# Kernel optimization log

Hardware: AMD Instinct MI355X
Metric: run time of the kernel (lower is better)

## Reference

```python
import jax, jax.numpy as jnp
import numpy as np

NUM_CODES = 1296
D_DIM = 64


def setup_inputs() -> dict:
    key = jax.random.key(0)
    k1, k2 = jax.random.split(key)
    inputs = jax.random.normal(k1, (32, 64, 64, D_DIM), dtype=jnp.float32)
    # lecun_normal init: stddev = 1/sqrt(fan_in) with fan_in = d
    embeddings = jax.random.normal(k2, (NUM_CODES, D_DIM), dtype=jnp.float32) / np.sqrt(D_DIM)
    return {"inputs": inputs, "embeddings": embeddings}


def reference(inputs, embeddings):
    x1 = jnp.sum(inputs ** 2, axis=-1, keepdims=True)          # [b,m,n,1]
    x2 = jnp.sum(embeddings ** 2, axis=-1)                      # [k]
    x3 = jnp.einsum('bmnd,kd->bmnk', inputs, embeddings)        # [b,m,n,k]
    D = x1 + x2 - 2.0 * x3
    codes = jnp.argmin(D, axis=-1).astype(jnp.int32)            # [b,m,n]
    code_vecs = embeddings[codes]                               # [b,m,n,d]
    return codes, code_vecs
```

## Files before the change

kernel.cpp:

```cpp
#include <hip/hip_runtime.h>

#define NUM_CODES 1296
#define PAD_CODES 1344
#define DDIM 64
#define NUM_Q 131072
#define THREADS 256
#define QPW 32
#define QPB 128
#define MARGIN 0.25f
#define SLOTS 24
#define CHUNK 96
#define NSTEP 14

typedef __attribute__((ext_vector_type(8))) short bf16x8;
typedef __attribute__((ext_vector_type(4))) float f32x4;

__device__ __forceinline__ ushort f2bf(float f) {
    unsigned u = __float_as_uint(f);
    return (ushort)((u + 0x7fffu + ((u >> 16) & 1u)) >> 16);
}

__global__ __launch_bounds__(64) void vq_prep(const float* __restrict__ emb,
                                              float* __restrict__ enorm,
                                              ushort* __restrict__ eh) {
    int k = blockIdx.x * 64 + threadIdx.x;
    if (k >= PAD_CODES) return;
    int ks = k < NUM_CODES ? k : NUM_CODES - 1;
    const float* e = emb + (size_t)ks * DDIM;
    float f[DDIM];
#pragma unroll
    for (int i = 0; i < 16; ++i) {
        float4 v = *(const float4*)(e + 4 * i);
        f[4*i] = v.x; f[4*i+1] = v.y; f[4*i+2] = v.z; f[4*i+3] = v.w;
    }
    {
#pragma clang fp contract(off)
        float r8[8];
#pragma unroll
        for (int j = 0; j < 8; ++j) { float t = f[j] * f[j]; r8[j] = t; }
#pragma unroll
        for (int i = 1; i < 8; ++i) {
#pragma unroll
            for (int j = 0; j < 8; ++j) { float t = f[i*8+j] * f[i*8+j]; r8[j] += t; }
        }
        enorm[k] = ((r8[0]+r8[1])+(r8[2]+r8[3])) + ((r8[4]+r8[5])+(r8[6]+r8[7]));
    }
    ushort h[DDIM];
#pragma unroll
    for (int d = 0; d < DDIM; ++d) h[d] = f2bf(f[d]);
    uint* dh = (uint*)(eh + (size_t)k * DDIM);
#pragma unroll
    for (int s = 0; s < 8; ++s) {
        int ds = s ^ (k & 7);
#pragma unroll
        for (int j = 0; j < 4; ++j)
            dh[ds*4 + j] = (uint)h[s*8 + 2*j] | ((uint)h[s*8 + 2*j + 1] << 16);
    }
}

__global__ __launch_bounds__(256) void vq_xnorm(const float* __restrict__ x,
                                                float* __restrict__ xnorm) {
    int q = blockIdx.x * 256 + threadIdx.x;
    const float* r = x + (size_t)q * DDIM;
    float f[DDIM];
#pragma unroll
    for (int i = 0; i < 16; ++i) {
        float4 v = *(const float4*)(r + 4 * i);
        f[4*i] = v.x; f[4*i+1] = v.y; f[4*i+2] = v.z; f[4*i+3] = v.w;
    }
    {
#pragma clang fp contract(off)
        float r8[8];
#pragma unroll
        for (int j = 0; j < 8; ++j) { float t = f[j] * f[j]; r8[j] = t; }
#pragma unroll
        for (int i = 1; i < 8; ++i) {
#pragma unroll
            for (int j = 0; j < 8; ++j) { float t = f[i*8+j] * f[i*8+j]; r8[j] += t; }
        }
        xnorm[q] = ((r8[0]+r8[1])+(r8[2]+r8[3])) + ((r8[4]+r8[5])+(r8[6]+r8[7]));
    }
}

__global__ __launch_bounds__(THREADS) void vq_main(
        const float* __restrict__ x, const float* __restrict__ emb,
        const float* __restrict__ enorm_g, const float* __restrict__ xnorm,
        const ushort* __restrict__ eh, float* __restrict__ out) {
    __shared__ ushort sbuf[2][CHUNK * DDIM];
    __shared__ float sen[PAD_CODES];
    __shared__ ushort wq[4][QPW * SLOTS];
    __shared__ unsigned qcnt[4][QPW];
    __shared__ unsigned skk[4][QPW];

    const int tid  = threadIdx.x;
    const int lane = tid & 63;
    const int w    = tid >> 6;
    const int cl   = lane & 15;
    const int g    = lane >> 4;
    const long qw  = (long)blockIdx.x * QPB + w * QPW;

    if (lane < QPW) qcnt[w][lane] = 0;

    bf16x8 a00, a01, a10, a11;
    {
        const float* xp0 = x + (qw + cl) * DDIM + g * 8;
        const float* xp1 = xp0 + 16 * DDIM;
#pragma unroll
        for (int j = 0; j < 8; ++j) {
            a00[j] = (short)f2bf(xp0[j]);
            a01[j] = (short)f2bf(xp0[j + 32]);
            a10[j] = (short)f2bf(xp1[j]);
            a11[j] = (short)f2bf(xp1[j + 32]);
        }
    }

    float rmin0[4], rmin1[4];
#pragma unroll
    for (int r = 0; r < 4; ++r) { rmin0[r] = __builtin_inff(); rmin1[r] = __builtin_inff(); }

    const int slot0 = (g     ^ (cl & 7)) * 8;
    const int slot1 = ((g+4) ^ (cl & 7)) * 8;
    const f32x4 z4 = {0.f, 0.f, 0.f, 0.f};

    {
        const float4* src = (const float4*)eh;
        float4 s0 = src[tid], s1 = src[256 + tid], s2 = src[512 + tid];
        *(float4*)&sbuf[0][(size_t)tid * 8]         = s0;
        *(float4*)&sbuf[0][(size_t)(256 + tid) * 8] = s1;
        *(float4*)&sbuf[0][(size_t)(512 + tid) * 8] = s2;
        for (int i = tid; i < PAD_CODES; i += THREADS) sen[i] = enorm_g[i];
    }
    __syncthreads();

#define MFMA_TILE(T, D0, D1) { \
        const ushort* bp_ = &sbuf[cur][(size_t)((T) * 16 + cl) * DDIM]; \
        bf16x8 b0_ = *(const bf16x8*)(bp_ + slot0); \
        bf16x8 b1_ = *(const bf16x8*)(bp_ + slot1); \
        D0 = __builtin_amdgcn_mfma_f32_16x16x32_bf16(a00, b0_, z4, 0, 0, 0); \
        D1 = __builtin_amdgcn_mfma_f32_16x16x32_bf16(a10, b0_, z4, 0, 0, 0); \
        D0 = __builtin_amdgcn_mfma_f32_16x16x32_bf16(a01, b1_, D0, 0, 0, 0); \
        D1 = __builtin_amdgcn_mfma_f32_16x16x32_bf16(a11, b1_, D1, 0, 0, 0); }

#define SCORE_TILE(T, D0, D1) { \
        float en_ = sen[cb + (T) * 16 + cl]; \
        _Pragma("unroll") \
        for (int r = 0; r < 4; ++r) { \
            D0[r] = fmaf(-2.f, D0[r], en_); \
            D1[r] = fmaf(-2.f, D1[r], en_); \
            rmin0[r] = fminf(rmin0[r], D0[r]); \
            rmin1[r] = fminf(rmin1[r], D1[r]); } }

#define TEST_TILE(T, D0, D1) { \
        const int c_ = cb + (T) * 16 + cl; \
        if (c_ < NUM_CODES) { \
            _Pragma("unroll") \
            for (int r = 0; r < 4; ++r) { \
                if (D0[r] <= thr0[r]) { \
                    unsigned i_ = atomicAdd(&qcnt[w][g*4 + r], 1u); \
                    if (i_ < SLOTS) wq[w][(g*4 + r) * SLOTS + i_] = (ushort)c_; } \
                if (D1[r] <= thr1[r]) { \
                    unsigned i_ = atomicAdd(&qcnt[w][16 + g*4 + r], 1u); \
                    if (i_ < SLOTS) wq[w][(16 + g*4 + r) * SLOTS + i_] = (ushort)c_; } } } }

    int cur = 0;
    for (int s = 0; s < NSTEP; ++s) {
        float4 n0, n1, n2;
        const bool more = (s + 1 < NSTEP);
        if (more) {
            const float4* src = (const float4*)(eh + (size_t)(s + 1) * CHUNK * DDIM);
            n0 = src[tid]; n1 = src[256 + tid]; n2 = src[512 + tid];
        }
        const int cb = s * CHUNK;
        f32x4 d00, d01, d02, d03, d04, d05;
        f32x4 d10, d11, d12, d13, d14, d15;
        MFMA_TILE(0, d00, d10); MFMA_TILE(1, d01, d11); MFMA_TILE(2, d02, d12);
        MFMA_TILE(3, d03, d13); MFMA_TILE(4, d04, d14); MFMA_TILE(5, d05, d15);
        SCORE_TILE(0, d00, d10); SCORE_TILE(1, d01, d11); SCORE_TILE(2, d02, d12);
        SCORE_TILE(3, d03, d13); SCORE_TILE(4, d04, d14); SCORE_TILE(5, d05, d15);
#pragma unroll
        for (int m = 1; m < 16; m <<= 1) {
#pragma unroll
            for (int r = 0; r < 4; ++r) {
                rmin0[r] = fminf(rmin0[r], __shfl_xor(rmin0[r], m, 64));
                rmin1[r] = fminf(rmin1[r], __shfl_xor(rmin1[r], m, 64));
            }
        }
        float thr0[4], thr1[4];
#pragma unroll
        for (int r = 0; r < 4; ++r) { thr0[r] = rmin0[r] + MARGIN; thr1[r] = rmin1[r] + MARGIN; }
        if (more) {
            *(float4*)&sbuf[cur ^ 1][(size_t)tid * 8]         = n0;
            *(float4*)&sbuf[cur ^ 1][(size_t)(256 + tid) * 8] = n1;
            *(float4*)&sbuf[cur ^ 1][(size_t)(512 + tid) * 8] = n2;
        }
        __syncthreads();
        TEST_TILE(0, d00, d10); TEST_TILE(1, d01, d11); TEST_TILE(2, d02, d12);
        TEST_TILE(3, d03, d13); TEST_TILE(4, d04, d14); TEST_TILE(5, d05, d15);
        cur ^= 1;
    }

    auto exact_pk = [&](int c, long gq) -> unsigned long long {
        const float* xr = x + gq * DDIM;
        const float* er = emb + (size_t)c * DDIM;
        float dot = 0.f;
#pragma unroll
        for (int p4 = 0; p4 < 16; ++p4) {
            float4 xv = *(const float4*)(xr + 4 * p4);
            float4 ev = *(const float4*)(er + 4 * p4);
            dot = fmaf(xv.x, ev.x, dot); dot = fmaf(xv.y, ev.y, dot);
            dot = fmaf(xv.z, ev.z, dot); dot = fmaf(xv.w, ev.w, dot);
        }
        float dist = (xnorm[gq] + sen[c]) - 2.f * dot;
        unsigned u = __float_as_uint(dist);
        unsigned key = (u & 0x80000000u) ? ~u : (u | 0x80000000u);
        return ((unsigned long long)key << 32) | (unsigned)c;
    };

    const int grp = lane >> 3, gl = lane & 7;
#pragma unroll
    for (int qo = 0; qo < 4; ++qo) {
        const int ql = qo * 8 + grp;
        const long gq = qw + ql;
        const unsigned nq = qcnt[w][ql];
        unsigned long long pk = ~0ULL;
        if (nq <= SLOTS) {
            for (unsigned i = gl; i < nq; i += 8) {
                unsigned long long t = exact_pk((int)wq[w][ql * SLOTS + i], gq);
                if (t < pk) pk = t;
            }
        }
#pragma unroll
        for (int m = 1; m < 8; m <<= 1) {
            unsigned long long o = (unsigned long long)__shfl_xor((long long)pk, m, 64);
            if (o < pk) pk = o;
        }
        if (gl == 0 && nq <= SLOTS) {
            skk[w][ql] = (unsigned)pk;
            out[gq] = (float)(unsigned)pk;
        }
    }
    for (int ql = 0; ql < QPW; ++ql) {
        if (qcnt[w][ql] <= SLOTS) continue;
        const long gq = qw + ql;
        unsigned long long pk = ~0ULL;
        for (int t = 0; t < 21; ++t) {
            int c = lane + (t << 6);
            if (c < NUM_CODES) {
                unsigned long long tp = exact_pk(c, gq);
                if (tp < pk) pk = tp;
            }
        }
#pragma unroll
        for (int m = 1; m < 64; m <<= 1) {
            unsigned long long o = (unsigned long long)__shfl_xor((long long)pk, m, 64);
            if (o < pk) pk = o;
        }
        if (lane == 0) {
            skk[w][ql] = (unsigned)pk;
            out[gq] = (float)(unsigned)pk;
        }
    }

    const int gu = lane >> 4, gv = lane & 15;
#pragma unroll
    for (int qo = 0; qo < 8; ++qo) {
        const int ql = qo * 4 + gu;
        const unsigned kk = skk[w][ql];
        const long gq = qw + ql;
        *(float4*)(out + (long)NUM_Q + gq * DDIM + gv * 4) =
            *(const float4*)(emb + (size_t)kk * DDIM + gv * 4);
    }
}

extern "C" void kernel_launch(void* const* d_in, const int* in_sizes, int n_in,
                              void* d_out, int out_size, void* d_ws, size_t ws_size,
                              hipStream_t stream) {
    const float* x   = (const float*)d_in[0];
    const float* emb = (const float*)d_in[1];
    float*  enorm = (float*)d_ws;
    float*  xnorm = (float*)((char*)d_ws + 8192);
    ushort* eh    = (ushort*)((char*)d_ws + 532480);

    hipLaunchKernelGGL(vq_prep, dim3(PAD_CODES / 64), dim3(64), 0, stream,
                       emb, enorm, eh);
    hipLaunchKernelGGL(vq_xnorm, dim3(NUM_Q / 256), dim3(256), 0, stream,
                       x, xnorm);
    hipLaunchKernelGGL(vq_main, dim3(NUM_Q / QPB), dim3(THREADS), 0, stream,
                       x, emb, enorm, xnorm, eh, (float*)d_out);
}
```

Measured before the change: 129.8 us.

## Double block to 8 waves sharing each staged codebook chunk; drop shared enorm

```diff
diff --git a/kernel.cpp b/kernel.cpp
--- a/kernel.cpp
+++ b/kernel.cpp
@@ -4,11 +4,12 @@
 #define PAD_CODES 1344
 #define DDIM 64
 #define NUM_Q 131072
-#define THREADS 256
+#define THREADS 512
+#define WAVES 8
 #define QPW 32
-#define QPB 128
+#define QPB 256
 #define MARGIN 0.25f
-#define SLOTS 24
+#define SLOTS 16
 #define CHUNK 96
 #define NSTEP 14
 
@@ -87,10 +88,9 @@
         const float* __restrict__ enorm_g, const float* __restrict__ xnorm,
         const ushort* __restrict__ eh, float* __restrict__ out) {
     __shared__ ushort sbuf[2][CHUNK * DDIM];
-    __shared__ float sen[PAD_CODES];
-    __shared__ ushort wq[4][QPW * SLOTS];
-    __shared__ unsigned qcnt[4][QPW];
-    __shared__ unsigned skk[4][QPW];
+    __shared__ ushort wq[WAVES][QPW * SLOTS];
+    __shared__ unsigned qcnt[WAVES][QPW];
+    __shared__ unsigned skk[WAVES][QPW];
 
     const int tid  = threadIdx.x;
     const int lane = tid & 63;
@@ -124,11 +124,11 @@
 
     {
         const float4* src = (const float4*)eh;
-        float4 s0 = src[tid], s1 = src[256 + tid], s2 = src[512 + tid];
-        *(float4*)&sbuf[0][(size_t)tid * 8]         = s0;
-        *(float4*)&sbuf[0][(size_t)(256 + tid) * 8] = s1;
-        *(float4*)&sbuf[0][(size_t)(512 + tid) * 8] = s2;
-        for (int i = tid; i < PAD_CODES; i += THREADS) sen[i] = enorm_g[i];
+        float4 s0 = src[tid];
+        float4 s1;
+        if (tid < 256) s1 = src[512 + tid];
+        *(float4*)&sbuf[0][(size_t)tid * 8] = s0;
+        if (tid < 256) *(float4*)&sbuf[0][(size_t)(512 + tid) * 8] = s1;
     }
     __syncthreads();
 
@@ -142,7 +142,7 @@
         D1 = __builtin_amdgcn_mfma_f32_16x16x32_bf16(a11, b1_, D1, 0, 0, 0); }
 
 #define SCORE_TILE(T, D0, D1) { \
-        float en_ = sen[cb + (T) * 16 + cl]; \
+        float en_ = en[T]; \
         _Pragma("unroll") \
         for (int r = 0; r < 4; ++r) { \
             D0[r] = fmaf(-2.f, D0[r], en_); \
@@ -164,13 +164,18 @@
 
     int cur = 0;
     for (int s = 0; s < NSTEP; ++s) {
-        float4 n0, n1, n2;
+        float4 n0, n1;
         const bool more = (s + 1 < NSTEP);
         if (more) {
             const float4* src = (const float4*)(eh + (size_t)(s + 1) * CHUNK * DDIM);
-            n0 = src[tid]; n1 = src[256 + tid]; n2 = src[512 + tid];
+            n0 = src[tid];
+            if (tid < 256) n1 = src[512 + tid];
         }
         const int cb = s * CHUNK;
+        float en[6];
+#pragma unroll
+        for (int t = 0; t < 6; ++t) en[t] = enorm_g[cb + t * 16 + cl];
+
         f32x4 d00, d01, d02, d03, d04, d05;
         f32x4 d10, d11, d12, d13, d14, d15;
         MFMA_TILE(0, d00, d10); MFMA_TILE(1, d01, d11); MFMA_TILE(2, d02, d12);
@@ -189,9 +194,8 @@
 #pragma unroll
         for (int r = 0; r < 4; ++r) { thr0[r] = rmin0[r] + MARGIN; thr1[r] = rmin1[r] + MARGIN; }
         if (more) {
-            *(float4*)&sbuf[cur ^ 1][(size_t)tid * 8]         = n0;
-            *(float4*)&sbuf[cur ^ 1][(size_t)(256 + tid) * 8] = n1;
-            *(float4*)&sbuf[cur ^ 1][(size_t)(512 + tid) * 8] = n2;
+            *(float4*)&sbuf[cur ^ 1][(size_t)tid * 8] = n0;
+            if (tid < 256) *(float4*)&sbuf[cur ^ 1][(size_t)(512 + tid) * 8] = n1;
         }
         __syncthreads();
         TEST_TILE(0, d00, d10); TEST_TILE(1, d01, d11); TEST_TILE(2, d02, d12);
@@ -210,7 +214,7 @@
             dot = fmaf(xv.x, ev.x, dot); dot = fmaf(xv.y, ev.y, dot);
             dot = fmaf(xv.z, ev.z, dot); dot = fmaf(xv.w, ev.w, dot);
         }
-        float dist = (xnorm[gq] + sen[c]) - 2.f * dot;
+        float dist = (xnorm[gq] + enorm_g[c]) - 2.f * dot;
         unsigned u = __float_as_uint(dist);
         unsigned key = (u & 0x80000000u) ? ~u : (u | 0x80000000u);
         return ((unsigned long long)key << 32) | (unsigned)c;
```

New measurement: 149.4 us. +15.1%, slower.
